# Kernel optimization log

Measured on AMD Instinct MI355X. Metric: run time of the kernel, lower is better.

## Reference

```python
import jax, jax.numpy as jnp
import numpy as np

TEMPERATURE = 0.5
EPS = 1e-8  # torch F.cosine_similarity norm clamp
B, D = 4096, 768


def setup_inputs() -> dict:
    key = jax.random.key(0)
    k1, k2 = jax.random.split(key)
    return {
        "aug_hidden1": jax.random.normal(k1, (B, D), dtype=jnp.float32),
        "aug_hidden2": jax.random.normal(k2, (B, D), dtype=jnp.float32),
    }


def reference(aug_hidden1, aug_hidden2):
    b = aug_hidden1.shape[0]
    n = 2 * b
    h = jnp.concatenate([aug_hidden1, aug_hidden2], axis=0)  # [N, D]
    norm = jnp.maximum(jnp.linalg.norm(h, axis=1, keepdims=True), EPS)
    hn = h / norm
    # cosine-similarity matrix via GEMM (equivalent to broadcasted cosine_similarity)
    sim = jnp.matmul(hn, hn.T) / TEMPERATURE  # [N, N]
    idx = jnp.arange(n)
    pos = sim[idx, (idx + b) % n]  # positives: sim(i, i+B) and sim(i+B, i)
    # row logits = {positive} U {all entries except diagonal and pair} = all off-diagonal
    # entries, so CrossEntropy(label=0) == logsumexp(off-diagonal row) - positive
    sim_masked = jnp.where(jnp.eye(n, dtype=bool), -jnp.inf, sim)
    lse = jax.nn.logsumexp(sim_masked, axis=1)  # [N]
    return jnp.mean(lse - pos)
```

## Files before the change

### kernel.cpp

```cpp
#include <hip/hip_runtime.h>
#include <hip/hip_bf16.h>


#define B_SZ 4096
#define D_SZ 768
#define N_SZ 8192
#define ROWB 384
constexpr float INV_T = 2.0f;

typedef float f32x16 __attribute__((ext_vector_type(16)));
typedef int i32x8 __attribute__((ext_vector_type(8)));
typedef int i32x4 __attribute__((ext_vector_type(4)));
typedef __attribute__((address_space(1))) const unsigned int gu32;
typedef __attribute__((address_space(3))) unsigned int lu32;

__device__ inline void async16(const void* g, void* l) {
    __builtin_amdgcn_global_load_lds((gu32*)g, (lu32*)l, 16, 0, 0);
}

__device__ inline unsigned fp4_enc(float v) {
    float a = fabsf(v);
    unsigned c;
    if (a < 1.25f)      c = (a < 0.25f) ? 0u : (a < 0.75f) ? 1u : 2u;
    else if (a < 2.5f)  c = (a < 1.75f) ? 3u : 4u;
    else                c = (a < 3.5f) ? 5u : (a < 5.0f) ? 6u : 7u;
    return c | (v < 0.f ? 8u : 0u);
}

__global__ __launch_bounds__(256) void prep_k(const float* __restrict__ h1,
                                              const float* __restrict__ h2,
                                              unsigned char* __restrict__ hn4,
                                              float* __restrict__ pos,
                                              float* __restrict__ rowsum) {
    const int i = blockIdx.x * 4 + (threadIdx.x >> 6);
    const int lane = threadIdx.x & 63;
    const float4* a4 = (const float4*)(h1 + (size_t)i * D_SZ);
    const float4* b4 = (const float4*)(h2 + (size_t)i * D_SZ);
    float4 av[3], bv[3];
    float sa = 0.f, sb = 0.f, dt = 0.f;
#pragma unroll
    for (int j = 0; j < 3; ++j) {
        av[j] = a4[lane * 3 + j];
        bv[j] = b4[lane * 3 + j];
        sa += av[j].x * av[j].x + av[j].y * av[j].y + av[j].z * av[j].z + av[j].w * av[j].w;
        sb += bv[j].x * bv[j].x + bv[j].y * bv[j].y + bv[j].z * bv[j].z + bv[j].w * bv[j].w;
        dt += av[j].x * bv[j].x + av[j].y * bv[j].y + av[j].z * bv[j].z + av[j].w * bv[j].w;
    }
#pragma unroll
    for (int m = 1; m < 64; m <<= 1) {
        sa += __shfl_xor(sa, m, 64);
        sb += __shfl_xor(sb, m, 64);
        dt += __shfl_xor(dt, m, 64);
    }
    const float n1 = fmaxf(sqrtf(sa), 1e-8f), n2 = fmaxf(sqrtf(sb), 1e-8f);
    const float i1 = 1.0f / n1, i2 = 1.0f / n2;
    const float s1 = i1 * 16.0f, s2 = i2 * 16.0f;
    unsigned short* d1 = (unsigned short*)(hn4 + (size_t)i * ROWB);
    unsigned short* d2 = (unsigned short*)(hn4 + (size_t)(i + B_SZ) * ROWB);
#pragma unroll
    for (int j = 0; j < 3; ++j) {
        float va[4] = {av[j].x, av[j].y, av[j].z, av[j].w};
        float vb[4] = {bv[j].x, bv[j].y, bv[j].z, bv[j].w};
        unsigned u1 = 0, u2 = 0;
#pragma unroll
        for (int e = 0; e < 4; ++e) {
            u1 |= fp4_enc(va[e] * s1) << (4 * e);
            u2 |= fp4_enc(vb[e] * s2) << (4 * e);
        }
        d1[lane * 3 + j] = (unsigned short)u1;
        d2[lane * 3 + j] = (unsigned short)u2;
    }
    if (lane == 0) {
        float p = dt * i1 * i2 * INV_T;
        pos[i] = p;
        pos[i + B_SZ] = p;
        rowsum[i] = 0.f;
        rowsum[i + B_SZ] = 0.f;
    }
}

#define BM 128
#define BN 128
#define SLAB 4096
#define WINB 128
#define NWIN 3

__global__ __launch_bounds__(512) void gemm_reduce_k(const unsigned char* __restrict__ hn4,
                                                     float* __restrict__ rowsum) {
    __shared__ __align__(16) unsigned char As[4 * SLAB];
    __shared__ __align__(16) unsigned char Bs[4 * SLAB];
    const int b = blockIdx.x;
    int tx = (int)((sqrtf(8.0f * (float)b + 1.0f) - 1.0f) * 0.5f);
    while ((tx + 1) * (tx + 2) / 2 <= b) ++tx;
    while (tx * (tx + 1) / 2 > b) --tx;
    const int ty = b - tx * (tx + 1) / 2;
    const int rowBase = ty * BM;
    const int colBase = tx * BN;
    const bool diagBlk = (ty == tx);

    const int tid = threadIdx.x;
    const int wave = tid >> 6;
    const int lane = tid & 63;
    const int l32 = lane & 31;
    const int half = lane >> 5;
    const int ms = wave & 3;
    const int nh = wave >> 2;

    f32x16 acc[2];
#pragma unroll
    for (int nt = 0; nt < 2; ++nt)
#pragma unroll
        for (int j = 0; j < 16; ++j) acc[nt][j] = 0.f;

    const bool stB = wave >= 4;
    const int cg = (lane & 1) ^ ((lane >> 3) & 1);
    const unsigned char* gsrc =
        hn4 + (size_t)((stB ? colBase : rowBase) + ms * 32 + (lane >> 1)) * ROWB + cg * 16;
    unsigned char* ldst = (stB ? Bs : As) + ms * 1024;

    const int p = half ^ ((l32 >> 2) & 1);
    const int aOff = (ms * 32 + l32) * 32 + p * 16;
    const int bOff = (nh * 64 + l32) * 32 + p * 16;

    for (int w = 0; w < NWIN; ++w) {
        __syncthreads();
        const unsigned char* g0 = gsrc + w * WINB;
#pragma unroll
        for (int s = 0; s < 4; ++s)
            async16(g0 + s * 32, ldst + s * SLAB);
        __syncthreads();

#pragma unroll
        for (int s = 0; s < 4; ++s) {
            const unsigned char* Ab = As + s * SLAB;
            const unsigned char* Bb = Bs + s * SLAB;
            i32x4 al = *(const i32x4*)(Ab + aOff);
            i32x8 a = {al[0], al[1], al[2], al[3], 0, 0, 0, 0};
#pragma unroll
            for (int nt = 0; nt < 2; ++nt) {
                i32x4 bl = *(const i32x4*)(Bb + bOff + nt * 1024);
                i32x8 bf = {bl[0], bl[1], bl[2], bl[3], 0, 0, 0, 0};
                acc[nt] = __builtin_amdgcn_mfma_scale_f32_32x32x64_f8f6f4(
                    a, bf, acc[nt], 4, 4, 0, 0x7B7B7B7B, 0, 0x7B7B7B7B);
            }
        }
    }

    float rs[16];
#pragma unroll
    for (int j = 0; j < 16; ++j) rs[j] = 0.f;
#pragma unroll
    for (int nt = 0; nt < 2; ++nt) {
        const int col = colBase + nh * 64 + nt * 32 + l32;
        float cs = 0.f;
#pragma unroll
        for (int j = 0; j < 16; ++j) {
            int row = rowBase + ms * 32 + (j & 3) + 8 * (j >> 2) + 4 * half;
            float e = __expf(acc[nt][j] * INV_T);
            e = (diagBlk && row == col) ? 0.f : e;
            rs[j] += e;
            cs += e;
        }
        if (!diagBlk) {
            cs += __shfl_xor(cs, 32, 64);
            if (half == 0) atomicAdd(&rowsum[col], cs);
        }
    }
#pragma unroll
    for (int j = 0; j < 16; ++j) {
        float s = rs[j];
#pragma unroll
        for (int m = 1; m < 32; m <<= 1) s += __shfl_xor(s, m, 64);
        if (l32 == 0)
            atomicAdd(&rowsum[rowBase + ms * 32 + (j & 3) + 8 * (j >> 2) + 4 * half], s);
    }
}

__global__ __launch_bounds__(1024) void finalize_k(const float* __restrict__ rowsum,
                                                   const float* __restrict__ pos,
                                                   float* __restrict__ out) {
    __shared__ float red[16];
    const int t = threadIdx.x;
    const float4* rs4 = (const float4*)rowsum;
    const float4* ps4 = (const float4*)pos;
    float s = 0.f;
#pragma unroll
    for (int j = 0; j < 2; ++j) {
        float4 r = rs4[t * 2 + j];
        float4 p = ps4[t * 2 + j];
        s += (__logf(r.x) - p.x) + (__logf(r.y) - p.y) +
             (__logf(r.z) - p.z) + (__logf(r.w) - p.w);
    }
#pragma unroll
    for (int m = 1; m < 64; m <<= 1) s += __shfl_xor(s, m, 64);
    if ((t & 63) == 0) red[t >> 6] = s;
    __syncthreads();
    if (t == 0) {
        float tot = 0.f;
#pragma unroll
        for (int w = 0; w < 16; ++w) tot += red[w];
        out[0] = tot * (1.0f / (float)N_SZ);
    }
}

extern "C" void kernel_launch(void* const* d_in, const int* in_sizes, int n_in,
                              void* d_out, int out_size, void* d_ws, size_t ws_size,
                              hipStream_t stream) {
    const float* h1 = (const float*)d_in[0];
    const float* h2 = (const float*)d_in[1];
    float* out = (float*)d_out;

    char* ws = (char*)d_ws;
    unsigned char* hn4 = (unsigned char*)ws;
    float* pos    = (float*)(ws + (size_t)N_SZ * ROWB);
    float* rowsum = (float*)(ws + (size_t)N_SZ * ROWB + 32768);

    prep_k<<<B_SZ / 4, 256, 0, stream>>>(h1, h2, hn4, pos, rowsum);
    const int nTiles = N_SZ / BN;
    const int nBlocks = nTiles * (nTiles + 1) / 2;
    gemm_reduce_k<<<nBlocks, 512, 0, stream>>>(hn4, rowsum);
    finalize_k<<<1, 1024, 0, stream>>>(rowsum, pos, out);
}
```

Measured before the change: 120.6 us.

## Double-buffer FP4 K windows, remap block order, and aggregate row/col sums in LDS

The K loop is split into six 64-byte windows held in two LDS buffers, so the next window's async global-to-LDS copy is issued while MFMAs run on the current one. Block indices are permuted across eight groups to change tile scheduling order, and the temperature scaling is folded into the MFMA scale exponent so the per-element multiply before exp is dropped. Row and column partial sums are first combined in shared memory, cutting global atomics to one per row and one per column per block. The extra barriers per window and the LDS reduction step add some overhead.

```diff
diff --git a/kernel.cpp b/kernel.cpp
--- a/kernel.cpp
+++ b/kernel.cpp
@@ -80,22 +80,23 @@
 }
 
 #define BM 128
-#define BN 128
 #define SLAB 4096
-#define WINB 128
-#define NWIN 3
+#define WINB 64
+#define NWIN 6
+#define BUFS 8192
 
 __global__ __launch_bounds__(512) void gemm_reduce_k(const unsigned char* __restrict__ hn4,
                                                      float* __restrict__ rowsum) {
-    __shared__ __align__(16) unsigned char As[4 * SLAB];
-    __shared__ __align__(16) unsigned char Bs[4 * SLAB];
-    const int b = blockIdx.x;
+    __shared__ __align__(16) unsigned char As[2 * BUFS];
+    __shared__ __align__(16) unsigned char Bs[2 * BUFS];
+    const int b0 = blockIdx.x;
+    const int b = (b0 & 7) * 260 + (b0 >> 3);
     int tx = (int)((sqrtf(8.0f * (float)b + 1.0f) - 1.0f) * 0.5f);
     while ((tx + 1) * (tx + 2) / 2 <= b) ++tx;
     while (tx * (tx + 1) / 2 > b) --tx;
     const int ty = b - tx * (tx + 1) / 2;
     const int rowBase = ty * BM;
-    const int colBase = tx * BN;
+    const int colBase = tx * BM;
     const bool diagBlk = (ty == tx);
 
     const int tid = threadIdx.x;
@@ -122,57 +123,75 @@
     const int aOff = (ms * 32 + l32) * 32 + p * 16;
     const int bOff = (nh * 64 + l32) * 32 + p * 16;
 
+    async16(gsrc, ldst);
+    async16(gsrc + 32, ldst + SLAB);
+    __syncthreads();
+
     for (int w = 0; w < NWIN; ++w) {
-        __syncthreads();
-        const unsigned char* g0 = gsrc + w * WINB;
-#pragma unroll
-        for (int s = 0; s < 4; ++s)
-            async16(g0 + s * 32, ldst + s * SLAB);
-        __syncthreads();
-
-#pragma unroll
-        for (int s = 0; s < 4; ++s) {
-            const unsigned char* Ab = As + s * SLAB;
-            const unsigned char* Bb = Bs + s * SLAB;
-            i32x4 al = *(const i32x4*)(Ab + aOff);
+        const int buf = w & 1;
+        if (w + 1 < NWIN) {
+            const unsigned char* g0 = gsrc + (w + 1) * WINB;
+            unsigned char* l0 = ldst + (buf ^ 1) * BUFS;
+            async16(g0, l0);
+            async16(g0 + 32, l0 + SLAB);
+        }
+        const unsigned char* Ab = As + buf * BUFS;
+        const unsigned char* Bb = Bs + buf * BUFS;
+#pragma unroll
+        for (int s = 0; s < 2; ++s) {
+            i32x4 al = *(const i32x4*)(Ab + s * SLAB + aOff);
             i32x8 a = {al[0], al[1], al[2], al[3], 0, 0, 0, 0};
 #pragma unroll
             for (int nt = 0; nt < 2; ++nt) {
-                i32x4 bl = *(const i32x4*)(Bb + bOff + nt * 1024);
+                i32x4 bl = *(const i32x4*)(Bb + s * SLAB + bOff + nt * 1024);
                 i32x8 bf = {bl[0], bl[1], bl[2], bl[3], 0, 0, 0, 0};
                 acc[nt] = __builtin_amdgcn_mfma_scale_f32_32x32x64_f8f6f4(
-                    a, bf, acc[nt], 4, 4, 0, 0x7B7B7B7B, 0, 0x7B7B7B7B);
+                    a, bf, acc[nt], 4, 4, 0, 0x7C7C7C7C, 0, 0x7B7B7B7B);
             }
         }
-    }
-
+        __syncthreads();
+    }
+
+    float* rowS = (float*)As;
+    float* colS = (float*)(As + 1024);
     float rs[16];
 #pragma unroll
     for (int j = 0; j < 16; ++j) rs[j] = 0.f;
+    float csum[2] = {0.f, 0.f};
 #pragma unroll
     for (int nt = 0; nt < 2; ++nt) {
         const int col = colBase + nh * 64 + nt * 32 + l32;
-        float cs = 0.f;
 #pragma unroll
         for (int j = 0; j < 16; ++j) {
-            int row = rowBase + ms * 32 + (j & 3) + 8 * (j >> 2) + 4 * half;
-            float e = __expf(acc[nt][j] * INV_T);
+            const int row = rowBase + ms * 32 + (j & 3) + 8 * (j >> 2) + 4 * half;
+            float e = __expf(acc[nt][j]);
             e = (diagBlk && row == col) ? 0.f : e;
             rs[j] += e;
-            cs += e;
-        }
-        if (!diagBlk) {
-            cs += __shfl_xor(cs, 32, 64);
-            if (half == 0) atomicAdd(&rowsum[col], cs);
+            csum[nt] += e;
         }
     }
 #pragma unroll
     for (int j = 0; j < 16; ++j) {
-        float s = rs[j];
-#pragma unroll
-        for (int m = 1; m < 32; m <<= 1) s += __shfl_xor(s, m, 64);
-        if (l32 == 0)
-            atomicAdd(&rowsum[rowBase + ms * 32 + (j & 3) + 8 * (j >> 2) + 4 * half], s);
+#pragma unroll
+        for (int m = 1; m < 32; m <<= 1) rs[j] += __shfl_xor(rs[j], m, 64);
+    }
+    if (l32 == 0) {
+#pragma unroll
+        for (int j = 0; j < 16; ++j)
+            rowS[nh * 128 + ms * 32 + (j & 3) + 8 * (j >> 2) + 4 * half] = rs[j];
+    }
+#pragma unroll
+    for (int nt = 0; nt < 2; ++nt) {
+        float c = csum[nt] + __shfl_xor(csum[nt], 32, 64);
+        if (half == 0) colS[ms * 128 + nh * 64 + nt * 32 + l32] = c;
+    }
+    __syncthreads();
+    if (tid < 128) {
+        atomicAdd(&rowsum[rowBase + tid], rowS[tid] + rowS[128 + tid]);
+    } else if (tid < 256 && !diagBlk) {
+        const int c = tid - 128;
+        atomicAdd(&rowsum[colBase + c],
+                  colS[c] + colS[128 + c] + colS[256 + c] + colS[384 + c]);
     }
 }
 
@@ -216,7 +235,7 @@
     float* rowsum = (float*)(ws + (size_t)N_SZ * ROWB + 32768);
 
     prep_k<<<B_SZ / 4, 256, 0, stream>>>(h1, h2, hn4, pos, rowsum);
-    const int nTiles = N_SZ / BN;
+    const int nTiles = N_SZ / BM;
     const int nBlocks = nTiles * (nTiles + 1) / 2;
     gemm_reduce_k<<<nBlocks, 512, 0, stream>>>(hn4, rowsum);
     finalize_k<<<1, 1024, 0, stream>>>(rowsum, pos, out);
```

New measurement: 109.4 us. -9.3%, faster.
